# Optimization experiments

Measured on AMD Instinct MI355X. Metric: run time of the kernel, lower is better.

## Reference

```python
import jax, jax.numpy as jnp
import numpy as np

FP8_MAX = 448.0  # max representable magnitude of float8_e4m3fn


def act_quant(x, block_size):
    """Blockwise fp8 quantization along the last dim.
    x: [M, K] -> q: [M, K//bs, bs] fp8, scale: [M, K//bs, 1] fp32."""
    m, k = x.shape
    xb = x.reshape(m, k // block_size, block_size)
    amax = jnp.max(jnp.abs(xb), axis=-1, keepdims=True)
    scale = jnp.maximum(amax, 1e-4) / FP8_MAX
    q = (xb / scale).astype(jnp.float8_e4m3fn)
    return q, scale


def dequant(q, scale):
    # q: [M, K//bs, bs], scale: [M, K//bs, 1] -> [M, K] fp32
    return (q.astype(jnp.float32) * scale).reshape(q.shape[0], -1)


def setup_inputs() -> dict:
    key = jax.random.key(0)
    k1, k2 = jax.random.split(key)
    B, S, D, F = 16, 4096, 512, 512
    x = jax.random.normal(k1, (B, S, D), dtype=jnp.float32)
    # lecun_normal-style init: std = 1/sqrt(fan_in)
    kernel = jax.random.normal(k2, (D, F), dtype=jnp.float32) / np.sqrt(D)
    bias = jnp.zeros((F,), dtype=jnp.float32)
    return {"x": x, "kernel": kernel, "bias": bias, "block_size": 128}


def reference(x, kernel, bias, block_size):
    input_shape = x.shape
    x_flat = x.reshape(-1, input_shape[-1])  # [M, K]
    # blockwise fp8 quantize activations and kernel
    xq, xs = act_quant(x_flat, block_size)
    kq, ks = act_quant(kernel, block_size)
    # fp8 GEMM with dequant scales == dequant-then-matmul in exact math
    y = dequant(xq, xs) @ dequant(kq, ks)  # [M, F]
    y = y + bias
    return y.reshape(input_shape[:-1] + (kernel.shape[1],))
```

## Files before the change

kernel.cpp:

```cpp
#include <hip/hip_runtime.h>
#include <hip/hip_bf16.h>

typedef __attribute__((ext_vector_type(4))) float  floatx4;
typedef __attribute__((ext_vector_type(2))) float  floatx2;
typedef __attribute__((ext_vector_type(8))) __bf16 bf16x8;

#define FP8_MAX 448.0f

__device__ __forceinline__ floatx2 fp8_qdq2(float a, float b) {
    int p = __builtin_amdgcn_cvt_pk_fp8_f32(a, b, 0, false);
    return __builtin_amdgcn_cvt_pk_f32_fp8(p, false);
}

__device__ __forceinline__ unsigned int f2bf(float f) {
    union { __hip_bfloat16 h; unsigned short u; } cv;
    cv.h = __float2bfloat16(f);
    return (unsigned int)cv.u;
}

__device__ __forceinline__ void async_copy16(void* lds, const void* g) {
    __builtin_amdgcn_global_load_lds(
        (const __attribute__((address_space(1))) unsigned int*)g,
        (__attribute__((address_space(3))) unsigned int*)lds, 16, 0, 0);
}

__global__ void wdq_kernel(const float* __restrict__ W,
                           __hip_bfloat16* __restrict__ Wt) {
    const int D = 512, F = 512;
    int d = blockIdx.x;
    int t = threadIdx.x;
    float4 v = *reinterpret_cast<const float4*>(W + (size_t)d * F + t * 4);
    float am = fmaxf(fmaxf(fabsf(v.x), fabsf(v.y)), fmaxf(fabsf(v.z), fabsf(v.w)));
#pragma unroll
    for (int s = 16; s >= 1; s >>= 1) am = fmaxf(am, __shfl_xor(am, s));
    float scale = fmaxf(am, 1e-4f) / FP8_MAX;
    floatx2 d01 = fp8_qdq2(v.x / scale, v.y / scale);
    floatx2 d23 = fp8_qdq2(v.z / scale, v.w / scale);
    int f0 = t * 4;
    Wt[(size_t)(f0 + 0) * D + d] = __float2bfloat16(d01[0] * scale);
    Wt[(size_t)(f0 + 1) * D + d] = __float2bfloat16(d01[1] * scale);
    Wt[(size_t)(f0 + 2) * D + d] = __float2bfloat16(d23[0] * scale);
    Wt[(size_t)(f0 + 3) * D + d] = __float2bfloat16(d23[1] * scale);
}

__global__ __launch_bounds__(256, 2) void fused_gemm(
        const float* __restrict__ X,
        const __hip_bfloat16* __restrict__ Wt,
        const float* __restrict__ bias,
        float* __restrict__ C, int M) {
    const int K = 512, N = 512;
    __shared__ char As[2][8192];
    __shared__ char Bs[2][32768];

    int bx   = blockIdx.x;
    int tile = (bx & 7) * (gridDim.x >> 3) + (bx >> 3);
    int tN   = tile & 1;
    int tM   = tile >> 1;

    int tid = threadIdx.x, wid = tid >> 6, lane = tid & 63;
    int wn = wid;
    int lr = lane & 15, lg = lane >> 4;
    int ar = tid >> 2, aq = tid & 3;

    const float* Xb = X + (size_t)(tM * 64) * K;
    const char* Wb  = (const char*)(Wt + (size_t)tN * 256 * K);
    float* Cb = C + (size_t)(tM * 64) * N + tN * 256;

    float4 vA[8], vB[8];
    uint4  q4[4];
    floatx4 acc[4][4] = {};

    auto loadX = [&](float4 (&v)[8], int qb) {
        const float* src = Xb + (size_t)ar * K + qb * 128 + aq * 32;
#pragma unroll
        for (int j = 0; j < 8; ++j)
            v[j] = *reinterpret_cast<const float4*>(src + j * 4);
    };
    auto quantX = [&](const float4 (&v)[8]) {
        float am = 0.f;
#pragma unroll
        for (int j = 0; j < 8; ++j)
            am = fmaxf(am, fmaxf(fmaxf(fabsf(v[j].x), fabsf(v[j].y)),
                                 fmaxf(fabsf(v[j].z), fabsf(v[j].w))));
        am = fmaxf(am, __shfl_xor(am, 1));
        am = fmaxf(am, __shfl_xor(am, 2));
        am = fmaxf(am, 1e-4f);
        float scale = am / FP8_MAX;
        float inv   = FP8_MAX / am;
#pragma unroll
        for (int n = 0; n < 4; ++n) {
            floatx2 a0 = fp8_qdq2(v[2*n].x*inv,   v[2*n].y*inv);
            floatx2 a1 = fp8_qdq2(v[2*n].z*inv,   v[2*n].w*inv);
            floatx2 a2 = fp8_qdq2(v[2*n+1].x*inv, v[2*n+1].y*inv);
            floatx2 a3 = fp8_qdq2(v[2*n+1].z*inv, v[2*n+1].w*inv);
            q4[n].x = f2bf(a0[0]*scale) | (f2bf(a0[1]*scale) << 16);
            q4[n].y = f2bf(a1[0]*scale) | (f2bf(a1[1]*scale) << 16);
            q4[n].z = f2bf(a2[0]*scale) | (f2bf(a2[1]*scale) << 16);
            q4[n].w = f2bf(a3[0]*scale) | (f2bf(a3[1]*scale) << 16);
        }
    };
    auto writeA = [&](int buf, int hb) {
        if ((aq >> 1) == hb) {
#pragma unroll
            for (int n = 0; n < 4; ++n) {
                int slot = (aq & 1) * 4 + n;
                *reinterpret_cast<uint4*>(
                    As[buf] + ar * 128 + ((slot ^ (ar & 7)) << 4)) = q4[n];
            }
        }
    };
    auto stageB = [&](int buf, int step) {
        const char* base = Wb + step * 128;
#pragma unroll
        for (int cc = 0; cc < 8; ++cc) {
            int c  = wid * 8 + cc;
            int rr = c * 8 + (lane >> 3);
            int d  = lane & 7;
            async_copy16(Bs[buf] + c * 1024,
                         base + (size_t)rr * (K * 2) + ((d ^ (rr & 7)) << 4));
        }
    };
    auto mfmaStep = [&](int buf) {
#pragma unroll
        for (int ks = 0; ks < 2; ++ks) {
            int q = (ks << 2) | lg;
            bf16x8 a[4], b[4];
#pragma unroll
            for (int mi = 0; mi < 4; ++mi) {
                int r = mi * 16 + lr;
                a[mi] = *reinterpret_cast<const bf16x8*>(
                    As[buf] + r * 128 + ((q ^ (r & 7)) << 4));
            }
#pragma unroll
            for (int ni = 0; ni < 4; ++ni) {
                int f = wn * 64 + ni * 16 + lr;
                b[ni] = *reinterpret_cast<const bf16x8*>(
                    Bs[buf] + f * 128 + ((q ^ (f & 7)) << 4));
            }
#pragma unroll
            for (int mi = 0; mi < 4; ++mi)
#pragma unroll
                for (int ni = 0; ni < 4; ++ni)
                    acc[mi][ni] = __builtin_amdgcn_mfma_f32_16x16x32_bf16(
                        a[mi], b[ni], acc[mi][ni], 0, 0, 0);
        }
    };
    auto boundary = [&](int n) {
        if (n == 8) asm volatile("s_waitcnt vmcnt(8)" ::: "memory");
        else        asm volatile("s_waitcnt vmcnt(0)" ::: "memory");
        asm volatile("s_waitcnt lgkmcnt(0)" ::: "memory");
        __builtin_amdgcn_s_barrier();
    };

    float bv[4];
#pragma unroll
    for (int ni = 0; ni < 4; ++ni)
        bv[ni] = bias[tN * 256 + wn * 64 + ni * 16 + lr];
    loadX(vA, 0);
    stageB(0, 0);
    __builtin_amdgcn_sched_barrier(0);
    loadX(vB, 1);
    quantX(vA);
    writeA(0, 0);
    boundary(8);

    stageB(1, 1);
    __builtin_amdgcn_sched_barrier(0);
    loadX(vA, 2);
    writeA(1, 1);
    mfmaStep(0);
    boundary(8);

    stageB(0, 2);
    quantX(vB);
    writeA(0, 0);
    mfmaStep(1);
    boundary(0);

    stageB(1, 3);
    __builtin_amdgcn_sched_barrier(0);
    loadX(vB, 3);
    writeA(1, 1);
    mfmaStep(0);
    boundary(8);

    stageB(0, 4);
    quantX(vA);
    writeA(0, 0);
    mfmaStep(1);
    boundary(0);

    stageB(1, 5);
    writeA(1, 1);
    mfmaStep(0);
    boundary(0);

    stageB(0, 6);
    quantX(vB);
    writeA(0, 0);
    mfmaStep(1);
    boundary(0);

    stageB(1, 7);
    writeA(1, 1);
    mfmaStep(0);
    boundary(0);

    mfmaStep(1);

#pragma unroll
    for (int ni = 0; ni < 4; ++ni) {
        int col = wn * 64 + ni * 16 + lr;
#pragma unroll
        for (int mi = 0; mi < 4; ++mi) {
            int r0 = mi * 16 + lg * 4;
#pragma unroll
            for (int e = 0; e < 4; ++e)
                Cb[(size_t)(r0 + e) * N + col] = acc[mi][ni][e] + bv[ni];
        }
    }
}

extern "C" void kernel_launch(void* const* d_in, const int* in_sizes, int n_in,
                              void* d_out, int out_size, void* d_ws, size_t ws_size,
                              hipStream_t stream) {
    const float* X    = (const float*)d_in[0];
    const float* W    = (const float*)d_in[1];
    const float* bias = (const float*)d_in[2];
    const int K = 512;
    const int M = in_sizes[0] / K;

    __hip_bfloat16* Wt = (__hip_bfloat16*)d_ws;

    wdq_kernel<<<dim3(512), dim3(128), 0, stream>>>(W, Wt);
    fused_gemm<<<dim3((M / 64) * (512 / 256)), dim3(256), 0, stream>>>(
        X, Wt, bias, (float*)d_out, M);
}
```

Before: 86.56 us.

## Process four M tiles per block with cross-tile prefetch pipelining

Each workgroup now handles four consecutive 64-row M tiles instead of one, and the launch grid shrinks by the same factor. While the current tile's last k-steps run, the next tile's first X chunks are loaded and quantized. The previous tile's output stores are issued alongside the next tile's B staging. The aim is to amortize the per-block prologue and epilogue and to keep the MFMA pipeline busy across tile boundaries. In exchange, the grid has fewer blocks, which can hurt tail balance. The in-flight stores also enter the vmcnt accounting, so the waits may drain longer.

```diff
diff --git a/kernel.cpp b/kernel.cpp
--- a/kernel.cpp
+++ b/kernel.cpp
@@ -6,6 +6,7 @@
 typedef __attribute__((ext_vector_type(8))) __bf16 bf16x8;
 
 #define FP8_MAX 448.0f
+#define JOBS 4
 
 __device__ __forceinline__ floatx2 fp8_qdq2(float a, float b) {
     int p = __builtin_amdgcn_cvt_pk_fp8_f32(a, b, 0, false);
@@ -55,23 +56,23 @@
     int bx   = blockIdx.x;
     int tile = (bx & 7) * (gridDim.x >> 3) + (bx >> 3);
     int tN   = tile & 1;
-    int tM   = tile >> 1;
+    int mg   = tile >> 1;
 
     int tid = threadIdx.x, wid = tid >> 6, lane = tid & 63;
     int wn = wid;
     int lr = lane & 15, lg = lane >> 4;
     int ar = tid >> 2, aq = tid & 3;
 
-    const float* Xb = X + (size_t)(tM * 64) * K;
+    const float* Xb = X + (size_t)(mg * JOBS * 64) * K;
     const char* Wb  = (const char*)(Wt + (size_t)tN * 256 * K);
-    float* Cb = C + (size_t)(tM * 64) * N + tN * 256;
+    float* Cb = C + (size_t)(mg * JOBS * 64) * N + tN * 256;
 
     float4 vA[8], vB[8];
     uint4  q4[4];
     floatx4 acc[4][4] = {};
 
-    auto loadX = [&](float4 (&v)[8], int qb) {
-        const float* src = Xb + (size_t)ar * K + qb * 128 + aq * 32;
+    auto loadX = [&](float4 (&v)[8], const float* base, int qb) {
+        const float* src = base + (size_t)ar * K + qb * 128 + aq * 32;
 #pragma unroll
         for (int j = 0; j < 8; ++j)
             v[j] = *reinterpret_cast<const float4*>(src + j * 4);
@@ -145,6 +146,25 @@
                         a[mi], b[ni], acc[mi][ni], 0, 0, 0);
         }
     };
+    float bv[4];
+    auto storeC = [&](float* cb) {
+#pragma unroll
+        for (int ni = 0; ni < 4; ++ni) {
+            int col = wn * 64 + ni * 16 + lr;
+#pragma unroll
+            for (int mi = 0; mi < 4; ++mi) {
+                int r0 = mi * 16 + lg * 4;
+#pragma unroll
+                for (int e = 0; e < 4; ++e)
+                    cb[(size_t)(r0 + e) * N + col] = acc[mi][ni][e] + bv[ni];
+            }
+        }
+#pragma unroll
+        for (int mi = 0; mi < 4; ++mi)
+#pragma unroll
+            for (int ni = 0; ni < 4; ++ni)
+                acc[mi][ni] = floatx4{0.f, 0.f, 0.f, 0.f};
+    };
     auto boundary = [&](int n) {
         if (n == 8) asm volatile("s_waitcnt vmcnt(8)" ::: "memory");
         else        asm volatile("s_waitcnt vmcnt(0)" ::: "memory");
@@ -152,71 +172,80 @@
         __builtin_amdgcn_s_barrier();
     };
 
-    float bv[4];
 #pragma unroll
     for (int ni = 0; ni < 4; ++ni)
         bv[ni] = bias[tN * 256 + wn * 64 + ni * 16 + lr];
-    loadX(vA, 0);
+
+    loadX(vA, Xb, 0);
     stageB(0, 0);
     __builtin_amdgcn_sched_barrier(0);
-    loadX(vB, 1);
+    loadX(vB, Xb, 1);
     quantX(vA);
     writeA(0, 0);
     boundary(8);
 
-    stageB(1, 1);
-    __builtin_amdgcn_sched_barrier(0);
-    loadX(vA, 2);
-    writeA(1, 1);
-    mfmaStep(0);
-    boundary(8);
-
-    stageB(0, 2);
-    quantX(vB);
-    writeA(0, 0);
-    mfmaStep(1);
-    boundary(0);
-
-    stageB(1, 3);
-    __builtin_amdgcn_sched_barrier(0);
-    loadX(vB, 3);
-    writeA(1, 1);
-    mfmaStep(0);
-    boundary(8);
-
-    stageB(0, 4);
-    quantX(vA);
-    writeA(0, 0);
-    mfmaStep(1);
-    boundary(0);
-
-    stageB(1, 5);
-    writeA(1, 1);
-    mfmaStep(0);
-    boundary(0);
-
-    stageB(0, 6);
-    quantX(vB);
-    writeA(0, 0);
-    mfmaStep(1);
-    boundary(0);
-
-    stageB(1, 7);
-    writeA(1, 1);
-    mfmaStep(0);
-    boundary(0);
-
-    mfmaStep(1);
-
-#pragma unroll
-    for (int ni = 0; ni < 4; ++ni) {
-        int col = wn * 64 + ni * 16 + lr;
-#pragma unroll
-        for (int mi = 0; mi < 4; ++mi) {
-            int r0 = mi * 16 + lg * 4;
-#pragma unroll
-            for (int e = 0; e < 4; ++e)
-                Cb[(size_t)(r0 + e) * N + col] = acc[mi][ni][e] + bv[ni];
+#pragma unroll
+    for (int j = 0; j < JOBS; ++j) {
+        const float* Xn = Xb + (size_t)(j + 1) * 64 * K;
+
+        if (j > 0) storeC(Cb + (size_t)(j - 1) * 64 * N);
+        stageB(1, 1);
+        __builtin_amdgcn_sched_barrier(0);
+        loadX(vA, Xb + (size_t)j * 64 * K, 2);
+        writeA(1, 1);
+        mfmaStep(0);
+        boundary(8);
+
+        stageB(0, 2);
+        quantX(vB);
+        writeA(0, 0);
+        mfmaStep(1);
+        boundary(0);
+
+        stageB(1, 3);
+        __builtin_amdgcn_sched_barrier(0);
+        loadX(vB, Xb + (size_t)j * 64 * K, 3);
+        writeA(1, 1);
+        mfmaStep(0);
+        boundary(8);
+
+        stageB(0, 4);
+        quantX(vA);
+        writeA(0, 0);
+        mfmaStep(1);
+        boundary(0);
+
+        stageB(1, 5);
+        writeA(1, 1);
+        mfmaStep(0);
+        boundary(0);
+
+        stageB(0, 6);
+        quantX(vB);
+        writeA(0, 0);
+        mfmaStep(1);
+        boundary(0);
+
+        stageB(1, 7);
+        if (j < JOBS - 1) {
+            __builtin_amdgcn_sched_barrier(0);
+            loadX(vA, Xn, 0);
+        }
+        writeA(1, 1);
+        mfmaStep(0);
+        boundary(j < JOBS - 1 ? 8 : 0);
+
+        if (j < JOBS - 1) {
+            quantX(vA);
+            writeA(0, 0);
+            stageB(0, 0);
+            __builtin_amdgcn_sched_barrier(0);
+            loadX(vB, Xn, 1);
+            mfmaStep(1);
+            boundary(8);
+        } else {
+            mfmaStep(1);
+            storeC(Cb + (size_t)j * 64 * N);
         }
     }
 }
@@ -233,6 +262,6 @@
     __hip_bfloat16* Wt = (__hip_bfloat16*)d_ws;
 
     wdq_kernel<<<dim3(512), dim3(128), 0, stream>>>(W, Wt);
-    fused_gemm<<<dim3((M / 64) * (512 / 256)), dim3(256), 0, stream>>>(
+    fused_gemm<<<dim3((M / (64 * JOBS)) * (512 / 256)), dim3(256), 0, stream>>>(
         X, Wt, bias, (float*)d_out, M);
 }
```

Measured after the change: 150.2 us. +73.5%, slower.
